# Kernel optimization log

Hardware: AMD Instinct MI355X
Metric: run time of the kernel (lower is better)

## Reference

```python
import jax, jax.numpy as jnp
import numpy as np

T, N, D, E = 4, 50000, 32, 800000
V_TH = 1.0      # v_threshold
ALPHA = 4.0     # surrogate-gradient sharpness


def setup_inputs() -> dict:
    key = jax.random.key(0)
    k1, k2, k3, k4 = jax.random.split(key, 4)
    s_seq = jax.random.normal(k1, (T, N, D), dtype=jnp.float32) * 0.5
    z_seq = jax.random.normal(k2, (N, D), dtype=jnp.float32) * 0.5
    edge_index = jax.random.randint(k3, (2, E), 0, N, dtype=jnp.int64)
    # GCNConv weight (bias=False), Glorot-ish scale
    W = jax.random.normal(k4, (D, D), dtype=jnp.float32) / np.sqrt(D).astype(np.float32)
    return {"s_seq": s_seq, "z_seq": z_seq, "W": W, "edge_index": edge_index}


def _gcn_conv(x, W, edge_index, n_nodes):
    """PyG GCNConv with add_self_loops=True, normalize=True, bias=False.
    x: [T,N,D]; returns [T,N,D]."""
    src, dst = edge_index[0], edge_index[1]
    ones = jnp.ones(src.shape[0], dtype=x.dtype)
    deg = jax.ops.segment_sum(ones, dst, num_segments=n_nodes) + 1.0  # +1 self loop
    dinv = jax.lax.rsqrt(deg)                                        # [N]
    xw = jnp.einsum('tnd,df->tnf', x, W)                             # dense transform
    norm = dinv[src] * dinv[dst]                                     # [E]
    msgs = xw[:, src, :] * norm[None, :, None]                       # [T,E,D] gather
    agg = jax.vmap(lambda m: jax.ops.segment_sum(m, dst, num_segments=n_nodes))(msgs)
    # self-loop contribution with norm dinv[i]^2
    return agg + xw * (dinv * dinv)[None, :, None]


def _spike(v):
    # Heaviside spike with surrogate (sigmoid) gradient, straight-through.
    s = (v >= V_TH).astype(v.dtype)
    sg = jax.nn.sigmoid(ALPHA * (v - V_TH))
    return s + sg - jax.lax.stop_gradient(sg)


def reference(s_seq, z_seq, W, edge_index):
    n_nodes = s_seq.shape[1]
    x_seq = _gcn_conv(s_seq, W, edge_index, n_nodes)   # [T,N,D]  (dropout p=0.0 is identity)
    y_seq = x_seq.mean(0)                              # temporal mean [N,D]
    # Riemannian IF node: integrate-and-fire over time with soft reset;
    # latent state z drifts by the temporal mean (Euclidean proxy for expmap).
    def step(v, x_t):
        v = v + x_t
        o = _spike(v)
        v = v - o * V_TH
        return v, o
    v0 = jnp.zeros_like(z_seq)
    _, o_seq = jax.lax.scan(step, v0, x_seq)           # [T,N,D]
    z_new = z_seq + y_seq
    return o_seq, z_new
```

## Files before the change

### kernel.cpp

```cpp
#include <hip/hip_runtime.h>
#include <hip/hip_fp16.h>

#define TSTEPS 4
#define DIM 32
#define BINW_SHIFT 8
#define NB 256
#define SP_CH 2048
#define PAD_PER_BIN 772

typedef _Float16 f16x8 __attribute__((ext_vector_type(8)));
typedef float f32x4 __attribute__((ext_vector_type(4)));

__device__ __forceinline__ void ldx8h(const __half* p, float4& lo, float4& hi) {
    uint4 u = *(const uint4*)p;
    __half2 h0 = *(__half2*)&u.x;
    __half2 h1 = *(__half2*)&u.y;
    __half2 h2 = *(__half2*)&u.z;
    __half2 h3 = *(__half2*)&u.w;
    float2 a = __half22float2(h0);
    float2 b = __half22float2(h1);
    float2 c = __half22float2(h2);
    float2 d = __half22float2(h3);
    lo = make_float4(a.x, a.y, b.x, b.y);
    hi = make_float4(c.x, c.y, d.x, d.y);
}

__global__ __launch_bounds__(256) void deg_kernel(
    const int* __restrict__ ei, int* __restrict__ deg, int E) {
    int stride = gridDim.x * 256;
    for (int e = blockIdx.x * 256 + threadIdx.x; e < E; e += stride)
        atomicAdd(&deg[ei[E + e]], 1);
}

__global__ __launch_bounds__(256) void histgemm_kernel(
    const int* __restrict__ ei, int* __restrict__ ghist,
    const float* __restrict__ s, const float* __restrict__ W,
    const int* __restrict__ deg, __half* __restrict__ xwp,
    int E, int rows, int N, int nchunks) {
    __shared__ float Wf[32][33];
    int tid = threadIdx.x;

    if ((int)blockIdx.x < nchunks) {
        int* lh = (int*)Wf;
        lh[tid] = 0;
        __syncthreads();
        int beg = blockIdx.x * SP_CH;
        int end = min(beg + SP_CH, E);
        for (int e = beg + tid; e < end; e += 256)
            atomicAdd(&lh[ei[E + e] >> BINW_SHIFT], 1);
        __syncthreads();
        ghist[(size_t)blockIdx.x * NB + tid] = lh[tid];
        return;
    }

    {
        float4 wv = ((const float4*)W)[tid];
        int kk = tid >> 3, c4 = (tid & 7) * 4;
        Wf[kk][c4 + 0] = wv.x; Wf[kk][c4 + 1] = wv.y;
        Wf[kk][c4 + 2] = wv.z; Wf[kk][c4 + 3] = wv.w;
    }
    __syncthreads();

    int lane = tid & 63;
    int wid  = tid >> 6;
    int lrow = lane & 15;
    int kq   = lane >> 4;
    int k0   = kq * 8;

    f16x8 b0, b1;
#pragma unroll
    for (int i = 0; i < 8; i++) {
        b0[i] = (_Float16)Wf[k0 + i][lrow];
        b1[i] = (_Float16)Wf[k0 + i][lrow + 16];
    }

    int rbase = ((int)blockIdx.x - nchunks) * 128 + wid * 32;
#pragma unroll
    for (int rt = 0; rt < 2; rt++) {
        int r = rbase + rt * 16 + lrow;
        f16x8 a;
        if (r < rows) {
            const float4* sp = (const float4*)(s + (size_t)r * 32 + k0);
            float4 u0 = sp[0], u1 = sp[1];
            a[0] = (_Float16)u0.x; a[1] = (_Float16)u0.y;
            a[2] = (_Float16)u0.z; a[3] = (_Float16)u0.w;
            a[4] = (_Float16)u1.x; a[5] = (_Float16)u1.y;
            a[6] = (_Float16)u1.z; a[7] = (_Float16)u1.w;
        } else {
#pragma unroll
            for (int i = 0; i < 8; i++) a[i] = (_Float16)0.f;
        }
        f32x4 c0 = {0.f, 0.f, 0.f, 0.f};
        f32x4 c1 = {0.f, 0.f, 0.f, 0.f};
        c0 = __builtin_amdgcn_mfma_f32_16x16x32_f16(b0, a, c0, 0, 0, 0);
        c1 = __builtin_amdgcn_mfma_f32_16x16x32_f16(b1, a, c1, 0, 0, 0);
        if (r < rows) {
            int t = (r >= 3 * N) ? 3 : (r >= 2 * N) ? 2 : (r >= N) ? 1 : 0;
            int n = r - t * N;
            float di = rsqrtf((float)deg[n] + 1.0f);
            __half2 p0 = __floats2half2_rn(c0[0] * di, c0[1] * di);
            __half2 p1 = __floats2half2_rn(c0[2] * di, c0[3] * di);
            __half2 p2 = __floats2half2_rn(c1[0] * di, c1[1] * di);
            __half2 p3 = __floats2half2_rn(c1[2] * di, c1[3] * di);
            __half* dst = xwp + (size_t)n * 128 + t * 32;
            uint2 u0, u1;
            u0.x = *(unsigned int*)&p0; u0.y = *(unsigned int*)&p1;
            u1.x = *(unsigned int*)&p2; u1.y = *(unsigned int*)&p3;
            *(uint2*)(dst + kq * 4)      = u0;
            *(uint2*)(dst + 16 + kq * 4) = u1;
        }
    }
}

__global__ __launch_bounds__(512) void colscan_kernel(
    const int* __restrict__ ghist, int* __restrict__ ghist2,
    int* __restrict__ totals, int nchunks) {
    __shared__ int sc[512];
    int t = threadIdx.x;
    int b = blockIdx.x;
    int v = (t < nchunks) ? ghist[(size_t)t * NB + b] : 0;
    sc[t] = v;
    __syncthreads();
    for (int off = 1; off < 512; off <<= 1) {
        int tv = (t >= off) ? sc[t - off] : 0;
        __syncthreads();
        sc[t] += tv;
        __syncthreads();
    }
    if (t < nchunks) ghist2[(size_t)t * NB + b] = sc[t] - v;
    if (t == 511) totals[b] = sc[511];
}

__global__ __launch_bounds__(256) void split_kernel(
    const int* __restrict__ ei, const int* __restrict__ ghist,
    const int* __restrict__ ghist2, const int* __restrict__ totals,
    unsigned int* __restrict__ esorted, int E) {
    __shared__ int binB[NB], pscan[NB], gb[NB], pcur[NB];
    __shared__ unsigned int sbuf[SP_CH];
    int tid = threadIdx.x;
    int bid = blockIdx.x;

    int tot = totals[tid];
    binB[tid] = tot;
    __syncthreads();
    for (int off = 1; off < 256; off <<= 1) {
        int t = (tid >= off) ? binB[tid - off] : 0;
        __syncthreads();
        binB[tid] += t;
        __syncthreads();
    }
    int v = ghist[(size_t)bid * NB + tid];
    pscan[tid] = v;
    __syncthreads();
    for (int off = 1; off < 256; off <<= 1) {
        int t = (tid >= off) ? pscan[tid - off] : 0;
        __syncthreads();
        pscan[tid] += t;
        __syncthreads();
    }
    int pexcl = pscan[tid] - v;
    pscan[tid] = pexcl;
    pcur[tid] = pexcl;
    gb[tid] = (binB[tid] - tot) + ghist2[(size_t)bid * NB + tid] - pexcl;
    __syncthreads();

    int beg = bid * SP_CH;
    int end = min(beg + SP_CH, E);
    int cnt = end - beg;
    for (int e = beg + tid; e < end; e += 256) {
        int sx = ei[e];
        int dx = ei[E + e];
        unsigned int pk = (unsigned int)sx | ((unsigned int)dx << 16);
        int b = dx >> BINW_SHIFT;
        int p = atomicAdd(&pcur[b], 1);
        sbuf[p] = pk;
    }
    __syncthreads();
    for (int idx = tid; idx < cnt; idx += 256) {
        unsigned int e = sbuf[idx];
        int b = e >> 24;
        esorted[gb[b] + idx] = e;
    }
}

__global__ __launch_bounds__(256) void csr_kernel(
    const int* __restrict__ totals, const unsigned int* __restrict__ esorted,
    int* __restrict__ rec, int* __restrict__ offs,
    float* __restrict__ dinv, int N) {
    __shared__ int lh[NB], sc[NB], loff[NB], lcur[NB];
    __shared__ int s_ebeg, s_cnt;
    int bin = blockIdx.x;
    int tid = threadIdx.x;
    sc[tid] = totals[tid];
    lh[tid] = 0;
    __syncthreads();
    for (int off = 1; off < 256; off <<= 1) {
        int t = (tid >= off) ? sc[tid - off] : 0;
        __syncthreads();
        sc[tid] += t;
        __syncthreads();
    }
    if (tid == 0) {
        int e0 = bin ? sc[bin - 1] : 0;
        s_ebeg = e0;
        s_cnt = sc[bin] - e0;
    }
    __syncthreads();
    int ebeg = s_ebeg;
    int cnt = s_cnt;
    int gbase = ((ebeg + 3) & ~3) + PAD_PER_BIN * bin;
    for (int i = tid; i < cnt; i += 256)
        atomicAdd(&lh[(esorted[ebeg + i] >> 16) & 255], 1);
    __syncthreads();
    int padded = (lh[tid] + 3) & ~3;
    sc[tid] = padded;
    __syncthreads();
    for (int off = 1; off < 256; off <<= 1) {
        int t = (tid >= off) ? sc[tid - off] : 0;
        __syncthreads();
        sc[tid] += t;
        __syncthreads();
    }
    loff[tid] = sc[tid] - padded;
    lcur[tid] = 0;
    __syncthreads();
    for (int i = tid; i < cnt; i += 256) {
        unsigned int e = esorted[ebeg + i];
        int ln = (e >> 16) & 255;
        int p = atomicAdd(&lcur[ln], 1);
        rec[gbase + loff[ln] + p] = (int)(e & 0xFFFFu);
    }
    int n = (bin << BINW_SHIFT) + tid;
    if (n < N) {
        offs[n] = gbase + loff[tid];
        dinv[n] = rsqrtf((float)lh[tid] + 1.0f);
    }
}

__global__ __launch_bounds__(256) void gather_kernel(
    const int* __restrict__ rec, const int* __restrict__ offs,
    const int* __restrict__ deg, const __half* __restrict__ xwp,
    const float* __restrict__ dinv, const float* __restrict__ z,
    float* __restrict__ out, int N) {
    int gid = blockIdx.x * 256 + threadIdx.x;
    int n = gid >> 4;
    if (n >= N) return;
    int wl = threadIdx.x & 63;
    int g = wl >> 4;
    int l = wl & 15;
    long lofs = (long)l * 8;

    float dn = dinv[n];
    int beg = offs[n];
    int cntn = deg[n];

    float4 aLo = make_float4(0.f, 0.f, 0.f, 0.f);
    float4 aHi = make_float4(0.f, 0.f, 0.f, 0.f);
    int i = 0;
    for (; i + 8 <= cntn; i += 8) {
        int4 sa = *(const int4*)(rec + beg + i);
        int4 sb = *(const int4*)(rec + beg + i + 4);
        float4 l0, h0, l1, h1, l2, h2, l3, h3;
        float4 l4, h4, l5, h5, l6, h6, l7, h7;
        ldx8h(xwp + (long)sa.x * 128 + lofs, l0, h0);
        ldx8h(xwp + (long)sa.y * 128 + lofs, l1, h1);
        ldx8h(xwp + (long)sa.z * 128 + lofs, l2, h2);
        ldx8h(xwp + (long)sa.w * 128 + lofs, l3, h3);
        ldx8h(xwp + (long)sb.x * 128 + lofs, l4, h4);
        ldx8h(xwp + (long)sb.y * 128 + lofs, l5, h5);
        ldx8h(xwp + (long)sb.z * 128 + lofs, l6, h6);
        ldx8h(xwp + (long)sb.w * 128 + lofs, l7, h7);
        aLo.x += (l0.x + l1.x) + (l2.x + l3.x) + (l4.x + l5.x) + (l6.x + l7.x);
        aLo.y += (l0.y + l1.y) + (l2.y + l3.y) + (l4.y + l5.y) + (l6.y + l7.y);
        aLo.z += (l0.z + l1.z) + (l2.z + l3.z) + (l4.z + l5.z) + (l6.z + l7.z);
        aLo.w += (l0.w + l1.w) + (l2.w + l3.w) + (l4.w + l5.w) + (l6.w + l7.w);
        aHi.x += (h0.x + h1.x) + (h2.x + h3.x) + (h4.x + h5.x) + (h6.x + h7.x);
        aHi.y += (h0.y + h1.y) + (h2.y + h3.y) + (h4.y + h5.y) + (h6.y + h7.y);
        aHi.z += (h0.z + h1.z) + (h2.z + h3.z) + (h4.z + h5.z) + (h6.z + h7.z);
        aHi.w += (h0.w + h1.w) + (h2.w + h3.w) + (h4.w + h5.w) + (h6.w + h7.w);
    }
    for (; i < cntn; i += 4) {
        int4 s4 = *(const int4*)(rec + beg + i);
        int rem = cntn - i;
        int i0 = s4.x;
        int i1 = (rem > 1) ? s4.y : i0;
        int i2 = (rem > 2) ? s4.z : i0;
        int i3 = (rem > 3) ? s4.w : i0;
        float w1 = (rem > 1) ? 1.f : 0.f;
        float w2 = (rem > 2) ? 1.f : 0.f;
        float w3 = (rem > 3) ? 1.f : 0.f;
        float4 l0, h0, l1, h1, l2, h2, l3, h3;
        ldx8h(xwp + (long)i0 * 128 + lofs, l0, h0);
        ldx8h(xwp + (long)i1 * 128 + lofs, l1, h1);
        ldx8h(xwp + (long)i2 * 128 + lofs, l2, h2);
        ldx8h(xwp + (long)i3 * 128 + lofs, l3, h3);
        aLo.x += l0.x + w1 * l1.x + w2 * l2.x + w3 * l3.x;
        aLo.y += l0.y + w1 * l1.y + w2 * l2.y + w3 * l3.y;
        aLo.z += l0.z + w1 * l1.z + w2 * l2.z + w3 * l3.z;
        aLo.w += l0.w + w1 * l1.w + w2 * l2.w + w3 * l3.w;
        aHi.x += h0.x + w1 * h1.x + w2 * h2.x + w3 * h3.x;
        aHi.y += h0.y + w1 * h1.y + w2 * h2.y + w3 * h3.y;
        aHi.z += h0.z + w1 * h1.z + w2 * h2.z + w3 * h3.z;
        aHi.w += h0.w + w1 * h1.w + w2 * h2.w + w3 * h3.w;
    }
    {
        float4 sl, sh;
        ldx8h(xwp + (long)n * 128 + lofs, sl, sh);
        aLo.x += sl.x; aLo.y += sl.y; aLo.z += sl.z; aLo.w += sl.w;
        aHi.x += sh.x; aHi.y += sh.y; aHi.z += sh.z; aHi.w += sh.w;
    }
    aLo.x *= dn; aLo.y *= dn; aLo.z *= dn; aLo.w *= dn;
    aHi.x *= dn; aHi.y *= dn; aHi.z *= dn; aHi.w *= dn;

    float a8[8] = {aLo.x, aLo.y, aLo.z, aLo.w, aHi.x, aHi.y, aHi.z, aHi.w};
    float xs[TSTEPS][8];
    int base = g * 16;
#pragma unroll
    for (int t = 0; t < TSTEPS; t++) {
        int srcLane = base + t * 4 + l;
#pragma unroll
        for (int j = 0; j < 8; j++)
            xs[t][j] = __shfl(a8[j], srcLane, 64);
    }
    if (l < 4) {
        int colBase = n * 32 + l * 8;
        float v[8], y[8];
#pragma unroll
        for (int j = 0; j < 8; j++) {
            v[j] = 0.f;
            y[j] = (xs[0][j] + xs[1][j] + xs[2][j] + xs[3][j]) * 0.25f;
        }
#pragma unroll
        for (int t = 0; t < TSTEPS; t++) {
            float o[8];
#pragma unroll
            for (int j = 0; j < 8; j++) {
                v[j] += xs[t][j];
                o[j] = (v[j] >= 1.0f) ? 1.0f : 0.0f;
                v[j] -= o[j];
            }
            float* dst = out + (size_t)t * N * 32 + colBase;
            *(float4*)dst       = make_float4(o[0], o[1], o[2], o[3]);
            *(float4*)(dst + 4) = make_float4(o[4], o[5], o[6], o[7]);
        }
        float4 zv0 = *(const float4*)(z + colBase);
        float4 zv1 = *(const float4*)(z + colBase + 4);
        float* dst = out + (size_t)TSTEPS * N * 32 + colBase;
        *(float4*)dst       = make_float4(zv0.x + y[0], zv0.y + y[1], zv0.z + y[2], zv0.w + y[3]);
        *(float4*)(dst + 4) = make_float4(zv1.x + y[4], zv1.y + y[5], zv1.z + y[6], zv1.w + y[7]);
    }
}

extern "C" void kernel_launch(void* const* d_in, const int* in_sizes, int n_in,
                              void* d_out, int out_size, void* d_ws, size_t ws_size,
                              hipStream_t stream) {
    const float* s_seq = (const float*)d_in[0];
    const float* z_seq = (const float*)d_in[1];
    const float* W     = (const float*)d_in[2];
    const int*   ei    = (const int*)d_in[3];
    float* out = (float*)d_out;

    int N = in_sizes[1] / DIM;
    int E = in_sizes[3] / 2;
    int rows = TSTEPS * N;
    int nb = (N + 255) >> BINW_SHIFT;
    int nchunks = (E + SP_CH - 1) / SP_CH;

    char* w = (char*)d_ws;
    __half* xwp           = (__half*)w;       w += (size_t)rows * DIM * 2;
    unsigned int* esorted = (unsigned int*)w; w += (size_t)E * 4;
    int*   rec    = (int*)w;  w += ((size_t)E + PAD_PER_BIN * nb + 16) * 4;
    int*   offs   = (int*)w;  w += (size_t)N * 4;
    int*   deg    = (int*)w;  w += (size_t)N * 4;
    float* dinv   = (float*)w; w += (size_t)N * 4;
    int*   ghist  = (int*)w;  w += (size_t)nchunks * NB * 4;
    int*   ghist2 = (int*)w;  w += (size_t)nchunks * NB * 4;
    int*   totals = (int*)w;  w += NB * 4;

    hipMemsetAsync(deg, 0, (size_t)N * 4, stream);

    int xwBlocks = (rows + 127) / 128;
    deg_kernel<<<512, 256, 0, stream>>>(ei, deg, E);
    histgemm_kernel<<<nchunks + xwBlocks, 256, 0, stream>>>(
        ei, ghist, s_seq, W, deg, xwp, E, rows, N, nchunks);
    colscan_kernel<<<NB, 512, 0, stream>>>(ghist, ghist2, totals, nchunks);
    split_kernel<<<nchunks, 256, 0, stream>>>(ei, ghist, ghist2, totals, esorted, E);
    csr_kernel<<<nb, 256, 0, stream>>>(totals, esorted, rec, offs, dinv, N);
    gather_kernel<<<(N * 16 + 255) / 256, 256, 0, stream>>>(rec, offs, deg, xwp,
                                                            dinv, z_seq, out, N);
}
```

Baseline: 187.9 us.

## Drop separate degree kernel; derive degrees in CSR build and rescale xw there

Removes the memset and the atomic degree kernel. Degrees now come from the per-bin local histogram already built in csr_kernel, which writes deg and dinv and then rescales its 256-node slab of the fp16 xw buffer by dinv in place. This removes a full pass of global atomics over the edge list and a launch. In exchange it adds a read-modify-write of xwp (12.8 MB) inside csr_kernel and a second fp16 rounding step.

```diff
diff --git a/kernel.cpp b/kernel.cpp
--- a/kernel.cpp
+++ b/kernel.cpp
@@ -25,18 +25,10 @@
     hi = make_float4(c.x, c.y, d.x, d.y);
 }
 
-__global__ __launch_bounds__(256) void deg_kernel(
-    const int* __restrict__ ei, int* __restrict__ deg, int E) {
-    int stride = gridDim.x * 256;
-    for (int e = blockIdx.x * 256 + threadIdx.x; e < E; e += stride)
-        atomicAdd(&deg[ei[E + e]], 1);
-}
-
 __global__ __launch_bounds__(256) void histgemm_kernel(
     const int* __restrict__ ei, int* __restrict__ ghist,
     const float* __restrict__ s, const float* __restrict__ W,
-    const int* __restrict__ deg, __half* __restrict__ xwp,
-    int E, int rows, int N, int nchunks) {
+    __half* __restrict__ xwp, int E, int rows, int N, int nchunks) {
     __shared__ float Wf[32][33];
     int tid = threadIdx.x;
 
@@ -97,11 +89,10 @@
         if (r < rows) {
             int t = (r >= 3 * N) ? 3 : (r >= 2 * N) ? 2 : (r >= N) ? 1 : 0;
             int n = r - t * N;
-            float di = rsqrtf((float)deg[n] + 1.0f);
-            __half2 p0 = __floats2half2_rn(c0[0] * di, c0[1] * di);
-            __half2 p1 = __floats2half2_rn(c0[2] * di, c0[3] * di);
-            __half2 p2 = __floats2half2_rn(c1[0] * di, c1[1] * di);
-            __half2 p3 = __floats2half2_rn(c1[2] * di, c1[3] * di);
+            __half2 p0 = __floats2half2_rn(c0[0], c0[1]);
+            __half2 p1 = __floats2half2_rn(c0[2], c0[3]);
+            __half2 p2 = __floats2half2_rn(c1[0], c1[1]);
+            __half2 p3 = __floats2half2_rn(c1[2], c1[3]);
             __half* dst = xwp + (size_t)n * 128 + t * 32;
             uint2 u0, u1;
             u0.x = *(unsigned int*)&p0; u0.y = *(unsigned int*)&p1;
@@ -185,9 +176,10 @@
 
 __global__ __launch_bounds__(256) void csr_kernel(
     const int* __restrict__ totals, const unsigned int* __restrict__ esorted,
-    int* __restrict__ rec, int* __restrict__ offs,
-    float* __restrict__ dinv, int N) {
+    int* __restrict__ rec, int* __restrict__ offs, int* __restrict__ deg,
+    float* __restrict__ dinv, __half* __restrict__ xwp, int N) {
     __shared__ int lh[NB], sc[NB], loff[NB], lcur[NB];
+    __shared__ float sdi[NB];
     __shared__ int s_ebeg, s_cnt;
     int bin = blockIdx.x;
     int tid = threadIdx.x;
@@ -212,6 +204,7 @@
     for (int i = tid; i < cnt; i += 256)
         atomicAdd(&lh[(esorted[ebeg + i] >> 16) & 255], 1);
     __syncthreads();
+    sdi[tid] = rsqrtf((float)lh[tid] + 1.0f);
     int padded = (lh[tid] + 3) & ~3;
     sc[tid] = padded;
     __syncthreads();
@@ -233,7 +226,34 @@
     int n = (bin << BINW_SHIFT) + tid;
     if (n < N) {
         offs[n] = gbase + loff[tid];
-        dinv[n] = rsqrtf((float)lh[tid] + 1.0f);
+        deg[n] = lh[tid];
+        dinv[n] = sdi[tid];
+    }
+    {
+        int hbase = bin << 15;
+        int limit = min(32768, N * 128 - hbase);
+        __half* slab = xwp + hbase;
+        for (int i = tid; i * 8 < limit; i += 256) {
+            float di = sdi[i >> 4];
+            uint4 u = *(uint4*)(slab + i * 8);
+            __half2 h0 = *(__half2*)&u.x;
+            __half2 h1 = *(__half2*)&u.y;
+            __half2 h2 = *(__half2*)&u.z;
+            __half2 h3 = *(__half2*)&u.w;
+            float2 f0 = __half22float2(h0);
+            float2 f1 = __half22float2(h1);
+            float2 f2 = __half22float2(h2);
+            float2 f3 = __half22float2(h3);
+            h0 = __floats2half2_rn(f0.x * di, f0.y * di);
+            h1 = __floats2half2_rn(f1.x * di, f1.y * di);
+            h2 = __floats2half2_rn(f2.x * di, f2.y * di);
+            h3 = __floats2half2_rn(f3.x * di, f3.y * di);
+            u.x = *(unsigned int*)&h0;
+            u.y = *(unsigned int*)&h1;
+            u.z = *(unsigned int*)&h2;
+            u.w = *(unsigned int*)&h3;
+            *(uint4*)(slab + i * 8) = u;
+        }
     }
 }
 
@@ -377,15 +397,12 @@
     int*   ghist2 = (int*)w;  w += (size_t)nchunks * NB * 4;
     int*   totals = (int*)w;  w += NB * 4;
 
-    hipMemsetAsync(deg, 0, (size_t)N * 4, stream);
-
     int xwBlocks = (rows + 127) / 128;
-    deg_kernel<<<512, 256, 0, stream>>>(ei, deg, E);
     histgemm_kernel<<<nchunks + xwBlocks, 256, 0, stream>>>(
-        ei, ghist, s_seq, W, deg, xwp, E, rows, N, nchunks);
+        ei, ghist, s_seq, W, xwp, E, rows, N, nchunks);
     colscan_kernel<<<NB, 512, 0, stream>>>(ghist, ghist2, totals, nchunks);
     split_kernel<<<nchunks, 256, 0, stream>>>(ei, ghist, ghist2, totals, esorted, E);
-    csr_kernel<<<nb, 256, 0, stream>>>(totals, esorted, rec, offs, dinv, N);
+    csr_kernel<<<nb, 256, 0, stream>>>(totals, esorted, rec, offs, deg, dinv, xwp, N);
     gather_kernel<<<(N * 16 + 255) / 256, 256, 0, stream>>>(rec, offs, deg, xwp,
                                                             dinv, z_seq, out, N);
 }
```

New measurement: 154.2 us. 17.9% less time.
